# Kernel optimization log

Hardware: AMD Instinct MI355X
Metric: run time of the kernel (lower is better)

## Reference

```python
import jax, jax.numpy as jnp
import numpy as np

B, TQ, TKV, D, H = 2, 1024, 1024, 1024, 16
HD = D // H
BUCKETS, MAX_REL = 32, 128
SPAN = BUCKETS  # pos_ebd_size


def make_log_bucket_position(rel_pos, bucket_size, max_position):
    sign = jnp.sign(rel_pos)
    mid = bucket_size // 2
    abs_pos = jnp.where((rel_pos < mid) & (rel_pos > -mid), mid - 1, jnp.abs(rel_pos))
    log_pos = jnp.ceil(jnp.log(abs_pos.astype(jnp.float32) / mid)
                       / np.float32(np.log((max_position - 1) / mid)) * (mid - 1)) + mid
    return jnp.where(abs_pos <= mid, rel_pos, (log_pos * sign).astype(rel_pos.dtype))


def setup_inputs():
    key = jax.random.key(0)
    ks = jax.random.split(key, 12)
    s = 0.02
    f32 = jnp.float32
    return {
        "query_states": jax.random.normal(ks[0], (B, TQ, D), f32),
        "key_value_states": jax.random.normal(ks[1], (B, TKV, D), f32),
        "Wq": jax.random.normal(ks[2], (D, D), f32) * s, "bq": jnp.zeros((D,), f32),
        "Wk": jax.random.normal(ks[3], (D, D), f32) * s, "bk": jnp.zeros((D,), f32),
        "Wv": jax.random.normal(ks[4], (D, D), f32) * s, "bv": jnp.zeros((D,), f32),
        "Wo": jax.random.normal(ks[5], (D, D), f32) * s, "bo": jnp.zeros((D,), f32),
        "Wpk": jax.random.normal(ks[6], (D, D), f32) * s, "bpk": jnp.zeros((D,), f32),
        "Wpq": jax.random.normal(ks[7], (D, D), f32) * s, "bpq": jnp.zeros((D,), f32),
        "rel_emb": jax.random.normal(ks[8], (2 * SPAN, D), f32) * s,
        "ln_g": jnp.ones((D,), f32), "ln_b": jnp.zeros((D,), f32),
        "attention_mask": jnp.zeros((B, TKV), jnp.bool_),
    }


def reference(query_states, key_value_states, Wq, bq, Wk, bk, Wv, bv, Wo, bo,
              Wpk, bpk, Wpq, bpq, rel_emb, ln_g, ln_b, attention_mask):
    # projections -> [B,H,T,hd]
    q = (query_states @ Wq.T + bq).reshape(B, TQ, H, HD).transpose(0, 2, 1, 3)
    k = (key_value_states @ Wk.T + bk).reshape(B, TKV, H, HD).transpose(0, 2, 1, 3)
    v = (key_value_states @ Wv.T + bv).reshape(B, TKV, H, HD).transpose(0, 2, 1, 3)
    scale = jnp.sqrt(jnp.float32(HD * 3))  # scale_factor = 1 + c2p + p2c
    scores = jnp.einsum('bhqd,bhkd->bhqk', q, k) / scale

    # layer-normalized relative embeddings [2*SPAN, D]
    mu = rel_emb.mean(-1, keepdims=True)
    var = ((rel_emb - mu) ** 2).mean(-1, keepdims=True)
    re = (rel_emb - mu) * jax.lax.rsqrt(var + 1e-5) * ln_g + ln_b
    pos_k = (re @ Wpk.T + bpk).reshape(2 * SPAN, H, HD).transpose(1, 0, 2)  # [H,2S,hd]
    pos_q = (re @ Wpq.T + bpq).reshape(2 * SPAN, H, HD).transpose(1, 0, 2)

    rel = make_log_bucket_position(jnp.arange(TQ)[:, None] - jnp.arange(TKV)[None, :],
                                   BUCKETS, MAX_REL)                      # [Tq,Tkv]
    c2p_pos = jnp.clip(rel + SPAN, 0, 2 * SPAN - 1)
    p2c_pos = jnp.clip(-rel + SPAN, 0, 2 * SPAN - 1)
    pscale = jnp.sqrt(jnp.float32(HD * 2))

    # c2p: gather along relative-position axis
    c2p = jnp.einsum('bhqd,hpd->bhqp', q, pos_k)                          # [B,H,Tq,2S]
    iq = jnp.arange(TQ)[:, None]
    c2p_g = c2p[:, :, iq, c2p_pos]                                        # [B,H,Tq,Tkv]

    # p2c: gather then transpose (requires Tq == Tkv, as in original torch expand)
    p2c = jnp.einsum('bhkd,hpd->bhkp', k, pos_q)                          # [B,H,Tkv,2S]
    ik = jnp.arange(TKV)[:, None]
    p2c_g = p2c[:, :, ik, p2c_pos].transpose(0, 1, 3, 2)                  # [B,H,Tq,Tkv]

    scores = scores + c2p_g / pscale + p2c_g / pscale
    scores = jnp.where(attention_mask[:, None, None, :], -jnp.inf, scores)
    probs = jax.nn.softmax(scores.astype(jnp.float32), axis=-1).astype(q.dtype)

    ctx = jnp.einsum('bhqk,bhkd->bhqd', probs, v).transpose(0, 2, 1, 3).reshape(B, TQ, D)
    return ctx @ Wo.T + bo
```

## Files before the change

kernel.cpp:

```cpp
#include <hip/hip_runtime.h>
#include <hip/hip_bf16.h>
#include <math.h>

#define B   2
#define TQ  1024
#define TKV 1024
#define D   1024
#define H   16
#define HD  64
#define P   64
#define SPAN 32

#define NEG_INF (-3.0e38f)

typedef __attribute__((ext_vector_type(8))) short bf16x8;
typedef __attribute__((ext_vector_type(4))) float f32x4;
typedef unsigned short ushort_t;

static constexpr size_t RE_OFF   = 0;
static constexpr size_t POSK_OFF = (size_t)64 * 1024;
static constexpr size_t POSQ_OFF = (size_t)128 * 1024;
static constexpr size_t FLOATS_END = (size_t)192 * 1024;
static constexpr size_t SHORT_BASE_BYTES = FLOATS_END * 4;
static constexpr size_t C2P_S  = 0;
static constexpr size_t P2C_S  = (size_t)2 * 1024 * 1024;
static constexpr size_t QH_S   = (size_t)4 * 1024 * 1024;
static constexpr size_t QL_S   = (size_t)6 * 1024 * 1024;
static constexpr size_t KH_S   = (size_t)8 * 1024 * 1024;
static constexpr size_t KL_S   = (size_t)10 * 1024 * 1024;
static constexpr size_t VTH_S  = (size_t)12 * 1024 * 1024;
static constexpr size_t VTL_S  = (size_t)14 * 1024 * 1024;
static constexpr size_t CTXH_S = (size_t)16 * 1024 * 1024;
static constexpr size_t CTXL_S = (size_t)18 * 1024 * 1024;
static constexpr size_t AKVH_S = (size_t)20 * 1024 * 1024;
static constexpr size_t AKVL_S = (size_t)22 * 1024 * 1024;
static constexpr size_t TAB_OFF_BYTES = SHORT_BASE_BYTES + (size_t)24 * 1024 * 1024 * 2;

__device__ __forceinline__ void split2(float x, unsigned short& h, unsigned short& l) {
  unsigned int u = __float_as_uint(x);
  h = (unsigned short)(u >> 16);
  float r = x - __uint_as_float(u & 0xffff0000u);
  unsigned int v = __float_as_uint(r);
  v += 0x7fffu + ((v >> 16) & 1u);
  l = (unsigned short)(v >> 16);
}

__device__ __forceinline__ unsigned short bf16rn(float x) {
  unsigned int v = __float_as_uint(x);
  v += 0x7fffu + ((v >> 16) & 1u);
  return (unsigned short)(v >> 16);
}

__device__ __forceinline__ float bf2f(unsigned short u) {
  return __uint_as_float(((unsigned int)u) << 16);
}

__global__ __launch_bounds__(256) void fused_pre(const float* __restrict__ kv,
    ushort_t* __restrict__ oh, ushort_t* __restrict__ ol,
    const float* __restrict__ re_in, const float* __restrict__ ln_g,
    const float* __restrict__ ln_b, float* __restrict__ re_out,
    unsigned char* __restrict__ tab) {
  const int bid = blockIdx.x;
  const int tid = threadIdx.x;
  if (bid < 1024) {
    size_t i = ((size_t)bid * 256 + tid) * 8;
    float4 a = *(const float4*)&kv[i];
    float4 b = *(const float4*)&kv[i + 4];
    float xs[8] = {a.x, a.y, a.z, a.w, b.x, b.y, b.z, b.w};
    bf16x8 th, tl;
    #pragma unroll
    for (int j = 0; j < 8; j++) {
      unsigned short hh, ll;
      split2(xs[j], hh, ll);
      th[j] = (short)hh; tl[j] = (short)ll;
    }
    *(bf16x8*)&oh[i] = th;
    *(bf16x8*)&ol[i] = tl;
  } else if (bid < 1088) {
    const int row = bid - 1024;
    const float* xr = re_in + (size_t)row * D;
    __shared__ float red[4];
    float s = 0.f;
    for (int i = tid; i < D; i += 256) s += xr[i];
    #pragma unroll
    for (int off = 32; off; off >>= 1) s += __shfl_down(s, off);
    if ((tid & 63) == 0) red[tid >> 6] = s;
    __syncthreads();
    float mu = (red[0] + red[1] + red[2] + red[3]) * (1.0f / D);
    __syncthreads();
    float vs = 0.f;
    for (int i = tid; i < D; i += 256) { float dd = xr[i] - mu; vs += dd * dd; }
    #pragma unroll
    for (int off = 32; off; off >>= 1) vs += __shfl_down(vs, off);
    if ((tid & 63) == 0) red[tid >> 6] = vs;
    __syncthreads();
    float var = (red[0] + red[1] + red[2] + red[3]) * (1.0f / D);
    float rs = rsqrtf(var + 1e-5f);
    for (int i = tid; i < D; i += 256)
      re_out[(size_t)row * D + i] = (xr[i] - mu) * rs * ln_g[i] + ln_b[i];
  } else {
    int i = (bid - 1088) * 256 + tid;
    if (i >= 2047) return;
    int d = i - 1023;
    int ad = d < 0 ? -d : d;
    int bucket;
    if (ad <= 16) {
      bucket = d;
    } else {
      double x = log((double)ad / 16.0) / log(127.0 / 16.0) * 15.0;
      double xr = floor(x + 0.5);
      double xc = (fabs(x - xr) < 1e-9) ? xr : ceil(x);
      int li = (int)xc + 16;
      bucket = (d > 0) ? li : -li;
    }
    int t = bucket + SPAN;
    t = t < 0 ? 0 : (t > 63 ? 63 : t);
    tab[i] = (unsigned char)t;
  }
}

__global__ __launch_bounds__(256) void gemm_pos(const float* __restrict__ A,
    const float* __restrict__ W0, const float* __restrict__ b0, float* __restrict__ C0,
    const float* __restrict__ W1, const float* __restrict__ b1, float* __restrict__ C1) {
  const float* W = blockIdx.z ? W1 : W0;
  const float* bias = blockIdx.z ? b1 : b0;
  float* C = blockIdx.z ? C1 : C0;

  __shared__ short sAh[64 * 32], sAl[64 * 32], sBh[64 * 32], sBl[64 * 32];
  const int t = threadIdx.x;
  const int bn = blockIdx.x * 64;
  const int wid = t >> 6, lane = t & 63;
  const int wr = wid >> 1, wc = wid & 1;
  const int fr = lane & 15, fo = (lane >> 4) * 8;
  const int srow = t >> 3, scol = (t & 7) * 4;

  f32x4 acc[2][2];
  #pragma unroll
  for (int i = 0; i < 2; i++)
    #pragma unroll
    for (int j = 0; j < 2; j++) acc[i][j] = (f32x4){0.f, 0.f, 0.f, 0.f};

  float4 rA[2], rW[2];
  auto ld = [&](int k0) {
    #pragma unroll
    for (int i = 0; i < 2; i++) {
      rA[i] = *(const float4*)&A[(size_t)(srow + 32 * i) * 1024 + k0 + scol];
      rW[i] = *(const float4*)&W[(size_t)(bn + srow + 32 * i) * 1024 + k0 + scol];
    }
  };
  ld(0);

  for (int k0 = 0; k0 < 1024; k0 += 32) {
    __syncthreads();
    #pragma unroll
    for (int i = 0; i < 2; i++) {
      int row = srow + 32 * i;
      unsigned short h0,h1,h2,h3,l0,l1,l2,l3;
      split2(rA[i].x,h0,l0); split2(rA[i].y,h1,l1); split2(rA[i].z,h2,l2); split2(rA[i].w,h3,l3);
      *(short4*)&sAh[row * 32 + scol] = make_short4((short)h0,(short)h1,(short)h2,(short)h3);
      *(short4*)&sAl[row * 32 + scol] = make_short4((short)l0,(short)l1,(short)l2,(short)l3);
      split2(rW[i].x,h0,l0); split2(rW[i].y,h1,l1); split2(rW[i].z,h2,l2); split2(rW[i].w,h3,l3);
      *(short4*)&sBh[row * 32 + scol] = make_short4((short)h0,(short)h1,(short)h2,(short)h3);
      *(short4*)&sBl[row * 32 + scol] = make_short4((short)l0,(short)l1,(short)l2,(short)l3);
    }
    if (k0 + 32 < 1024) ld(k0 + 32);
    __syncthreads();

    bf16x8 ah[2], al[2], bh[2], bl[2];
    #pragma unroll
    for (int mf = 0; mf < 2; mf++) {
      int r = (wr * 32 + mf * 16 + fr) * 32 + fo;
      ah[mf] = *(const bf16x8*)&sAh[r];
      al[mf] = *(const bf16x8*)&sAl[r];
    }
    #pragma unroll
    for (int nf = 0; nf < 2; nf++) {
      int r = (wc * 32 + nf * 16 + fr) * 32 + fo;
      bh[nf] = *(const bf16x8*)&sBh[r];
      bl[nf] = *(const bf16x8*)&sBl[r];
    }
    #pragma unroll
    for (int mf = 0; mf < 2; mf++)
      #pragma unroll
      for (int nf = 0; nf < 2; nf++) {
        acc[mf][nf] = __builtin_amdgcn_mfma_f32_16x16x32_bf16(ah[mf], bh[nf], acc[mf][nf], 0, 0, 0);
        acc[mf][nf] = __builtin_amdgcn_mfma_f32_16x16x32_bf16(ah[mf], bl[nf], acc[mf][nf], 0, 0, 0);
        acc[mf][nf] = __builtin_amdgcn_mfma_f32_16x16x32_bf16(al[mf], bh[nf], acc[mf][nf], 0, 0, 0);
      }
  }

  #pragma unroll
  for (int mf = 0; mf < 2; mf++) {
    int rbase = wr * 32 + mf * 16 + (lane >> 4) * 4;
    #pragma unroll
    for (int nf = 0; nf < 2; nf++) {
      int col = bn + wc * 32 + nf * 16 + fr;
      float bb = bias[col];
      #pragma unroll
      for (int r = 0; r < 4; r++)
        C[(size_t)(rbase + r) * 1024 + col] = acc[mf][nf][r] + bb;
    }
  }
}

__global__ __launch_bounds__(256) void gemm_split(
    const float* __restrict__ Aq,
    const ushort_t* __restrict__ AKVH, const ushort_t* __restrict__ AKVL,
    const float* __restrict__ W0, const float* __restrict__ W1, const float* __restrict__ W2,
    const float* __restrict__ b0, const float* __restrict__ b1, const float* __restrict__ b2,
    ushort_t* __restrict__ QH_, ushort_t* __restrict__ QL_,
    ushort_t* __restrict__ KH_, ushort_t* __restrict__ KL_,
    ushort_t* __restrict__ VH_, ushort_t* __restrict__ VL_,
    int K) {
  const int z = blockIdx.z;
  const float* W = (z == 0) ? W0 : (z == 1) ? W1 : W2;
  const float* bias = (z == 0) ? b0 : (z == 1) ? b1 : b2;

  const int flat2 = blockIdx.y * 16 + blockIdx.x;
  const int x = flat2 & 7, w = flat2 >> 3;
  const int bm = ((x >> 1) * 4 + (w >> 3)) * 128;
  const int bn = ((x & 1) * 8 + (w & 7)) * 64;

  __shared__ short sAhi[128 * 32];
  __shared__ short sAlo[128 * 32];
  __shared__ short sBhi[64 * 32];
  __shared__ short sBlo[64 * 32];

  const int t = threadIdx.x;
  const int wid = t >> 6, lane = t & 63;
  const int wr = wid >> 1, wc = wid & 1;
  const int fr = lane & 15, g = lane >> 4;

  f32x4 acc[4][2];
  #pragma unroll
  for (int i = 0; i < 4; i++)
    #pragma unroll
    for (int j = 0; j < 2; j++)
      acc[i][j] = (f32x4){0.f, 0.f, 0.f, 0.f};

  const int srow = t >> 3;
  const int scol = (t & 7) * 4;
  const int ar = t >> 1;
  const int ac = (t & 1) * 16;

  float4 rA[4], rW[2];
  bf16x8 rAH[2], rAL[2];
  auto ld = [&](int k0) {
    if (z == 0) {
      #pragma unroll
      for (int i = 0; i < 4; i++)
        rA[i] = *(const float4*)&Aq[(size_t)(bm + srow + 32 * i) * K + k0 + scol];
    } else {
      const size_t abase = (size_t)(bm + ar) * K + k0 + ac;
      rAH[0] = *(const bf16x8*)&AKVH[abase];
      rAH[1] = *(const bf16x8*)&AKVH[abase + 8];
      rAL[0] = *(const bf16x8*)&AKVL[abase];
      rAL[1] = *(const bf16x8*)&AKVL[abase + 8];
    }
    #pragma unroll
    for (int i = 0; i < 2; i++)
      rW[i] = *(const float4*)&W[(size_t)(bn + srow + 32 * i) * K + k0 + scol];
  };
  ld(0);

  for (int k0 = 0; k0 < K; k0 += 32) {
    __syncthreads();
    if (z == 0) {
      #pragma unroll
      for (int i = 0; i < 4; i++) {
        int row = srow + 32 * i;
        int dst = ((row >> 4) * 4 + (scol >> 3)) * 128 + (row & 15) * 8 + (scol & 7);
        unsigned short h0, h1, h2, h3, l0, l1, l2, l3;
        split2(rA[i].x, h0, l0); split2(rA[i].y, h1, l1); split2(rA[i].z, h2, l2); split2(rA[i].w, h3, l3);
        *(short4*)&sAhi[dst] = make_short4((short)h0, (short)h1, (short)h2, (short)h3);
        *(short4*)&sAlo[dst] = make_short4((short)l0, (short)l1, (short)l2, (short)l3);
      }
    } else {
      const int g0 = ac >> 3;
      const int base0 = ((ar >> 4) * 4 + g0) * 128 + (ar & 15) * 8;
      const int base1 = ((ar >> 4) * 4 + g0 + 1) * 128 + (ar & 15) * 8;
      *(bf16x8*)&sAhi[base0] = rAH[0];
      *(bf16x8*)&sAhi[base1] = rAH[1];
      *(bf16x8*)&sAlo[base0] = rAL[0];
      *(bf16x8*)&sAlo[base1] = rAL[1];
    }
    #pragma unroll
    for (int i = 0; i < 2; i++) {
      int row = srow + 32 * i;
      int dst = ((row >> 4) * 4 + (scol >> 3)) * 128 + (row & 15) * 8 + (scol & 7);
      unsigned short h0, h1, h2, h3, l0, l1, l2, l3;
      split2(rW[i].x, h0, l0); split2(rW[i].y, h1, l1); split2(rW[i].z, h2, l2); split2(rW[i].w, h3, l3);
      *(short4*)&sBhi[dst] = make_short4((short)h0, (short)h1, (short)h2, (short)h3);
      *(short4*)&sBlo[dst] = make_short4((short)l0, (short)l1, (short)l2, (short)l3);
    }
    if (k0 + 32 < K) ld(k0 + 32);
    __syncthreads();

    bf16x8 ah[4], al[4], bh[2], bl[2];
    #pragma unroll
    for (int mf = 0; mf < 4; mf++) {
      int r = ((wr * 4 + mf) * 4 + g) * 128 + fr * 8;
      ah[mf] = *(const bf16x8*)&sAhi[r];
      al[mf] = *(const bf16x8*)&sAlo[r];
    }
    #pragma unroll
    for (int nf = 0; nf < 2; nf++) {
      int r = ((wc * 2 + nf) * 4 + g) * 128 + fr * 8;
      bh[nf] = *(const bf16x8*)&sBhi[r];
      bl[nf] = *(const bf16x8*)&sBlo[r];
    }
    #pragma unroll
    for (int mf = 0; mf < 4; mf++)
      #pragma unroll
      for (int nf = 0; nf < 2; nf++) {
        acc[mf][nf] = __builtin_amdgcn_mfma_f32_16x16x32_bf16(ah[mf], bh[nf], acc[mf][nf], 0, 0, 0);
        acc[mf][nf] = __builtin_amdgcn_mfma_f32_16x16x32_bf16(ah[mf], bl[nf], acc[mf][nf], 0, 0, 0);
        acc[mf][nf] = __builtin_amdgcn_mfma_f32_16x16x32_bf16(al[mf], bh[nf], acc[mf][nf], 0, 0, 0);
      }
  }

  if (z == 2) {
    #pragma unroll
    for (int mf = 0; mf < 4; mf++) {
      int m0 = bm + wr * 64 + mf * 16 + (lane >> 4) * 4;
      int bb2 = m0 >> 10, t0 = m0 & 1023;
      #pragma unroll
      for (int nf = 0; nf < 2; nf++) {
        int col = bn + wc * 32 + nf * 16 + fr;
        int hh = col >> 6, dd = col & 63;
        float bvv = bias[col];
        unsigned short h4[4], l4[4];
        #pragma unroll
        for (int r = 0; r < 4; r++) split2(acc[mf][nf][r] + bvv, h4[r], l4[r]);
        size_t dst = (((size_t)bb2 * 16 + hh) * 64 + dd) * 1024 + t0;
        *(short4*)&VH_[dst] = make_short4((short)h4[0], (short)h4[1], (short)h4[2], (short)h4[3]);
        *(short4*)&VL_[dst] = make_short4((short)l4[0], (short)l4[1], (short)l4[2], (short)l4[3]);
      }
    }
  } else {
    ushort_t* OH = (z == 0) ? QH_ : KH_;
    ushort_t* OL = (z == 0) ? QL_ : KL_;
    #pragma unroll
    for (int mf = 0; mf < 4; mf++) {
      int rbase = bm + wr * 64 + mf * 16 + (lane >> 4) * 4;
      #pragma unroll
      for (int nf = 0; nf < 2; nf++) {
        int col = bn + wc * 32 + nf * 16 + fr;
        float bb = bias[col];
        #pragma unroll
        for (int r = 0; r < 4; r++) {
          unsigned short hh, ll;
          split2(acc[mf][nf][r] + bb, hh, ll);
          OH[(size_t)(rbase + r) * 1024 + col] = hh;
          OL[(size_t)(rbase + r) * 1024 + col] = ll;
        }
      }
    }
  }
}

__global__ __launch_bounds__(256) void gemm_out(
    const ushort_t* __restrict__ AH, const ushort_t* __restrict__ AL,
    const float* __restrict__ W, const float* __restrict__ bias, float* __restrict__ C) {
  __shared__ short sAh[64 * 32], sAl[64 * 32], sBh[64 * 32], sBl[64 * 32];
  const int t = threadIdx.x;
  const int flat2 = blockIdx.y * 16 + blockIdx.x;
  const int x = flat2 & 7, w = flat2 >> 3;
  const int bm = ((x >> 1) * 8 + (w >> 3)) * 64;
  const int bn = ((x & 1) * 8 + (w & 7)) * 64;
  const int wid = t >> 6, lane = t & 63;
  const int wr = wid >> 1, wc = wid & 1;
  const int fr = lane & 15, g = lane >> 4;
  const int arow = t >> 2, achk = (t & 3) * 8;
  const int srow = t >> 3, scol = (t & 7) * 4;

  f32x4 acc[2][2];
  #pragma unroll
  for (int i = 0; i < 2; i++)
    #pragma unroll
    for (int j = 0; j < 2; j++) acc[i][j] = (f32x4){0.f, 0.f, 0.f, 0.f};

  bf16x8 rAH, rAL;
  float4 rW[2];
  auto ld = [&](int k0) {
    rAH = *(const bf16x8*)&AH[(size_t)(bm + arow) * 1024 + k0 + achk];
    rAL = *(const bf16x8*)&AL[(size_t)(bm + arow) * 1024 + k0 + achk];
    #pragma unroll
    for (int i = 0; i < 2; i++)
      rW[i] = *(const float4*)&W[(size_t)(bn + srow + 32 * i) * 1024 + k0 + scol];
  };
  ld(0);

  for (int k0 = 0; k0 < 1024; k0 += 32) {
    __syncthreads();
    {
      const int dstA = ((arow >> 4) * 4 + (achk >> 3)) * 128 + (arow & 15) * 8;
      *(bf16x8*)&sAh[dstA] = rAH;
      *(bf16x8*)&sAl[dstA] = rAL;
    }
    #pragma unroll
    for (int i = 0; i < 2; i++) {
      int row = srow + 32 * i;
      int dst = ((row >> 4) * 4 + (scol >> 3)) * 128 + (row & 15) * 8 + (scol & 7);
      unsigned short h0,h1,h2,h3,l0,l1,l2,l3;
      split2(rW[i].x,h0,l0); split2(rW[i].y,h1,l1); split2(rW[i].z,h2,l2); split2(rW[i].w,h3,l3);
      *(short4*)&sBh[dst] = make_short4((short)h0,(short)h1,(short)h2,(short)h3);
      *(short4*)&sBl[dst] = make_short4((short)l0,(short)l1,(short)l2,(short)l3);
    }
    if (k0 + 32 < 1024) ld(k0 + 32);
    __syncthreads();

    bf16x8 ah[2], al[2], bh[2], bl[2];
    #pragma unroll
    for (int mf = 0; mf < 2; mf++) {
      int r = ((wr * 2 + mf) * 4 + g) * 128 + fr * 8;
      ah[mf] = *(const bf16x8*)&sAh[r];
      al[mf] = *(const bf16x8*)&sAl[r];
    }
    #pragma unroll
    for (int nf = 0; nf < 2; nf++) {
      int r = ((wc * 2 + nf) * 4 + g) * 128 + fr * 8;
      bh[nf] = *(const bf16x8*)&sBh[r];
      bl[nf] = *(const bf16x8*)&sBl[r];
    }
    #pragma unroll
    for (int mf = 0; mf < 2; mf++)
      #pragma unroll
      for (int nf = 0; nf < 2; nf++) {
        acc[mf][nf] = __builtin_amdgcn_mfma_f32_16x16x32_bf16(ah[mf], bh[nf], acc[mf][nf], 0, 0, 0);
        acc[mf][nf] = __builtin_amdgcn_mfma_f32_16x16x32_bf16(ah[mf], bl[nf], acc[mf][nf], 0, 0, 0);
        acc[mf][nf] = __builtin_amdgcn_mfma_f32_16x16x32_bf16(al[mf], bh[nf], acc[mf][nf], 0, 0, 0);
      }
  }

  #pragma unroll
  for (int mf = 0; mf < 2; mf++) {
    int rbase = bm + wr * 32 + mf * 16 + (lane >> 4) * 4;
    #pragma unroll
    for (int nf = 0; nf < 2; nf++) {
      int col = bn + wc * 32 + nf * 16 + fr;
      float bb = bias[col];
      #pragma unroll
      for (int r = 0; r < 4; r++)
        C[(size_t)(rbase + r) * 1024 + col] = acc[mf][nf][r] + bb;
    }
  }
}

__global__ __launch_bounds__(256) void relproj_mfma(
    const ushort_t* __restrict__ QH, const ushort_t* __restrict__ QL,
    const ushort_t* __restrict__ KH, const ushort_t* __restrict__ KL,
    const float* __restrict__ POSK, const float* __restrict__ POSQ,
    ushort_t* __restrict__ O0, ushort_t* __restrict__ O1) {
  const int z = blockIdx.z;
  const ushort_t* XH = z ? KH : QH;
  const ushort_t* XL = z ? KL : QL;
  const float* POS = z ? POSQ : POSK;
  ushort_t* out = z ? O1 : O0;
  const int bh = blockIdx.y, b = bh >> 4, h = bh & 15;
  const int t0 = blockIdx.x * 256;

  const int tid = threadIdx.x;
  const int wid = tid >> 6, lane = tid & 63;
  const int g = lane >> 4, fr = lane & 15;

  __shared__ __align__(16) short sPh[4096], sPl[4096];
  {
    const int sr = tid >> 2;
    const int cb = (tid & 3) * 16;
    const float* pp = &POS[(size_t)sr * 1024 + h * HD + cb];
    #pragma unroll
    for (int o = 0; o < 16; o += 8) {
      float4 a = *(const float4*)(pp + o);
      float4 c = *(const float4*)(pp + o + 4);
      float xs[8] = {a.x, a.y, a.z, a.w, c.x, c.y, c.z, c.w};
      bf16x8 th, tl;
      #pragma unroll
      for (int j = 0; j < 8; j++) {
        unsigned short hh, ll;
        split2(xs[j], hh, ll);
        th[j] = (short)hh; tl[j] = (short)ll;
      }
      int d0 = cb + o;
      int addr = (((sr >> 4) * 8) + ((d0 >> 5) * 4) + ((d0 >> 3) & 3)) * 128 + (sr & 15) * 8;
      *(bf16x8*)&sPh[addr] = th;
      *(bf16x8*)&sPl[addr] = tl;
    }
  }
  __syncthreads();

  const float inv_ps = 0.08838834764831845f;
  f32x4 acc[4][4];
  #pragma unroll
  for (int mf = 0; mf < 4; mf++)
    #pragma unroll
    for (int nf = 0; nf < 4; nf++) acc[mf][nf] = (f32x4){0.f, 0.f, 0.f, 0.f};

  #pragma unroll
  for (int mf = 0; mf < 4; mf++) {
    const int trow = t0 + wid * 64 + mf * 16 + fr;
    const size_t xbase = ((size_t)b * TQ + trow) * D + h * HD;
    #pragma unroll
    for (int ks = 0; ks < 2; ks++) {
      bf16x8 ah = *(const bf16x8*)&XH[xbase + ks * 32 + g * 8];
      bf16x8 al = *(const bf16x8*)&XL[xbase + ks * 32 + g * 8];
      #pragma unroll
      for (int nf = 0; nf < 4; nf++) {
        bf16x8 bhf = *(const bf16x8*)&sPh[(nf * 8 + ks * 4 + g) * 128 + fr * 8];
        bf16x8 blf = *(const bf16x8*)&sPl[(nf * 8 + ks * 4 + g) * 128 + fr * 8];
        acc[mf][nf] = __builtin_amdgcn_mfma_f32_16x16x32_bf16(ah, bhf, acc[mf][nf], 0, 0, 0);
        acc[mf][nf] = __builtin_amdgcn_mfma_f32_16x16x32_bf16(ah, blf, acc[mf][nf], 0, 0, 0);
        acc[mf][nf] = __builtin_amdgcn_mfma_f32_16x16x32_bf16(al, bhf, acc[mf][nf], 0, 0, 0);
      }
    }
  }

  #pragma unroll
  for (int mf = 0; mf < 4; mf++) {
    #pragma unroll
    for (int nf = 0; nf < 4; nf++) {
      int p = nf * 16 + fr;
      #pragma unroll
      for (int rr = 0; rr < 4; rr++) {
        int tt = t0 + wid * 64 + mf * 16 + g * 4 + rr;
        out[((size_t)bh * TQ + tt) * P + p] = bf16rn(acc[mf][nf][rr] * inv_ps);
      }
    }
  }
}

__global__ __launch_bounds__(256, 3) void attn_mfma(
    const ushort_t* __restrict__ QHB, const ushort_t* __restrict__ QLB,
    const ushort_t* __restrict__ KH, const ushort_t* __restrict__ KL,
    const ushort_t* __restrict__ VTH, const ushort_t* __restrict__ VTL,
    const ushort_t* __restrict__ c2p, const ushort_t* __restrict__ p2c,
    const unsigned char* __restrict__ mask, const unsigned char* __restrict__ tab,
    ushort_t* __restrict__ CTXH, ushort_t* __restrict__ CTXL) {
  const int flat = blockIdx.y * gridDim.x + blockIdx.x;
  const int nid = (flat & 7) * 64 + (flat >> 3);
  const int bh = nid >> 4, b = bh >> 4, h = bh & 15;
  const int q0 = (nid & 15) * 64;

  const int tid = threadIdx.x;
  const int wid = tid >> 6, lane = tid & 63;
  const int g = lane >> 4, fr = lane & 15;

  __shared__ __align__(16) short sKh[4096], sKl[4096], sVh[4096], sVl[4096];
  __shared__ __align__(16) ushort_t sc2p[64][72];
  __shared__ __align__(16) ushort_t sp2c[64][72];
  __shared__ unsigned char stab[384];
  __shared__ unsigned char smask[64];

  bf16x8 qh[2], ql[2];
  {
    const int qrow = q0 + wid * 16 + fr;
    const size_t qidx = ((size_t)b * TQ + qrow) * D + h * HD + g * 8;
    #pragma unroll
    for (int ks = 0; ks < 2; ks++) {
      qh[ks] = *(const bf16x8*)&QHB[qidx + ks * 32];
      ql[ks] = *(const bf16x8*)&QLB[qidx + ks * 32];
    }
  }

  const int sr = tid >> 2;
  const int sj0 = tid & 3;
  const int smf = sr >> 4, sfr = sr & 15;
  const int cb = (tid & 3) * 16;
  const int qloc = wid * 16 + fr;

  {
    const ushort_t* cp = c2p + ((size_t)bh * TQ + q0 + sr) * P + cb;
    *(bf16x8*)&sc2p[sr][cb]     = *(const bf16x8*)cp;
    *(bf16x8*)&sc2p[sr][cb + 8] = *(const bf16x8*)(cp + 8);
  }
  if (tid < 192) {
    stab[tid] = tab[832 + tid];
    stab[tid + 192] = (tid + 192 < 384) ? tab[832 + tid + 192] : (unsigned char)0;
  }
  __syncthreads();
  const float c2p0  = bf2f(sc2p[qloc][0]);
  const float c2p63 = bf2f(sc2p[qloc][63]);

  f32x4 acc[4];
  #pragma unroll
  for (int nf = 0; nf < 4; nf++) acc[nf] = (f32x4){0.f, 0.f, 0.f, 0.f};
  float m_run = NEG_INF, l_run = 0.f;

  const float inv_s = 0.07216878364870323f;

  bf16x8 rKh[2], rKl[2], rVh[2], rVl[2], rP0, rP1;
  unsigned char rmask = 0;

  auto load_tile = [&](int kt) {
    const int k0n = kt * 64;
    const size_t kbase = ((size_t)b * TKV + k0n + sr) * D + h * HD;
    const size_t vbase = ((size_t)bh * HD + sr) * TKV + k0n;
    const ushort_t* pp = p2c + ((size_t)bh * TKV + k0n + sr) * P + cb;
    #pragma unroll
    for (int u = 0; u < 2; u++) {
      int jj = sj0 + u * 4;
      rKh[u] = *(const bf16x8*)(KH + kbase + jj * 8);
      rKl[u] = *(const bf16x8*)(KL + kbase + jj * 8);
      rVh[u] = *(const bf16x8*)(VTH + vbase + jj * 8);
      rVl[u] = *(const bf16x8*)(VTL + vbase + jj * 8);
    }
    rP0 = *(const bf16x8*)pp;
    rP1 = *(const bf16x8*)(pp + 8);
    if (tid < 64) rmask = mask[(size_t)b * TKV + k0n + tid];
  };

  load_tile(0);

  for (int kt = 0; kt < TKV / 64; kt++) {
    const int k0 = kt * 64;
    __syncthreads();
    #pragma unroll
    for (int u = 0; u < 2; u++) {
      int jj = sj0 + u * 4;
      int sub = smf * 8 + (jj >> 2) * 4 + (jj & 3);
      *(bf16x8*)&sKh[sub * 128 + sfr * 8] = rKh[u];
      *(bf16x8*)&sKl[sub * 128 + sfr * 8] = rKl[u];
      *(bf16x8*)&sVh[sub * 128 + sfr * 8] = rVh[u];
      *(bf16x8*)&sVl[sub * 128 + sfr * 8] = rVl[u];
    }
    *(bf16x8*)&sp2c[sr][cb]     = rP0;
    *(bf16x8*)&sp2c[sr][cb + 8] = rP1;
    if (tid < 64) smask[tid] = rmask;
    if (kt + 1 < TKV / 64) load_tile(kt + 1);
    __syncthreads();

    f32x4 st[4];
    #pragma unroll
    for (int mf = 0; mf < 4; mf++) st[mf] = (f32x4){0.f, 0.f, 0.f, 0.f};
    __builtin_amdgcn_s_setprio(1);
    #pragma unroll
    for (int mf = 0; mf < 4; mf++) {
      #pragma unroll
      for (int ks = 0; ks < 2; ks++) {
        bf16x8 kh = *(const bf16x8*)&sKh[(mf * 8 + ks * 4 + g) * 128 + fr * 8];
        bf16x8 kl = *(const bf16x8*)&sKl[(mf * 8 + ks * 4 + g) * 128 + fr * 8];
        st[mf] = __builtin_amdgcn_mfma_f32_16x16x32_bf16(kh, qh[ks], st[mf], 0, 0, 0);
        st[mf] = __builtin_amdgcn_mfma_f32_16x16x32_bf16(kh, ql[ks], st[mf], 0, 0, 0);
        st[mf] = __builtin_amdgcn_mfma_f32_16x16x32_bf16(kl, qh[ks], st[mf], 0, 0, 0);
      }
    }
    __builtin_amdgcn_s_setprio(0);

    const int dtile = q0 - k0;
    float pv[4][4];
    float lmax = NEG_INF;
    if (dtile >= 192 || dtile <= -192) {
      const int C = (dtile >= 192) ? 63 : 0;
      const float cbias = (dtile >= 192) ? c2p63 : c2p0;
      #pragma unroll
      for (int mf = 0; mf < 4; mf++) {
        #pragma unroll
        for (int rr = 0; rr < 4; rr++) {
          int kj = mf * 16 + g * 4 + rr;
          float v = st[mf][rr] * inv_s + (cbias + bf2f(sp2c[kj][C]));
          v = smask[kj] ? NEG_INF : v;
          pv[mf][rr] = v;
          lmax = fmaxf(lmax, v);
        }
      }
    } else {
      const int dqs = q0 + qloc - k0 + 191;
      const ushort_t* c2prow = &sc2p[qloc][0];
      #pragma unroll
      for (int mf = 0; mf < 4; mf++) {
        #pragma unroll
        for (int rr = 0; rr < 4; rr++) {
          int kj = mf * 16 + g * 4 + rr;
          int tbi = stab[dqs - kj];
          float v = st[mf][rr] * inv_s + (bf2f(c2prow[tbi]) + bf2f(sp2c[kj][tbi]));
          v = smask[kj] ? NEG_INF : v;
          pv[mf][rr] = v;
          lmax = fmaxf(lmax, v);
        }
      }
    }
    lmax = fmaxf(lmax, __shfl_xor(lmax, 16));
    lmax = fmaxf(lmax, __shfl_xor(lmax, 32));
    if (!__all(lmax <= m_run)) {
      float mnew = fmaxf(m_run, lmax);
      float fac = __expf(m_run - mnew);
      m_run = mnew;
      l_run *= fac;
      float facr[4];
      #pragma unroll
      for (int rr = 0; rr < 4; rr++) facr[rr] = __shfl(fac, g * 4 + rr);
      #pragma unroll
      for (int nf = 0; nf < 4; nf++)
        #pragma unroll
        for (int rr = 0; rr < 4; rr++) acc[nf][rr] *= facr[rr];
    }
    float psum = 0.f;
    #pragma unroll
    for (int mf = 0; mf < 4; mf++)
      #pragma unroll
      for (int rr = 0; rr < 4; rr++) {
        float e = __expf(pv[mf][rr] - m_run);
        pv[mf][rr] = e;
        psum += e;
      }
    psum += __shfl_xor(psum, 16);
    psum += __shfl_xor(psum, 32);
    l_run += psum;

    bf16x8 pa[2];
    #pragma unroll
    for (int ks = 0; ks < 2; ks++) {
      bf16x8 t;
      #pragma unroll
      for (int j = 0; j < 8; j++) {
        int src = ((2 * (g & 1) + (j >> 2)) << 4) | fr;
        float v0 = __shfl(pv[2 * ks][j & 3], src);
        float v1 = __shfl(pv[2 * ks + 1][j & 3], src);
        float pvv = (g >> 1) ? v1 : v0;
        t[j] = (short)bf16rn(pvv);
      }
      pa[ks] = t;
    }

    __builtin_amdgcn_s_setprio(1);
    #pragma unroll
    for (int nf = 0; nf < 4; nf++) {
      #pragma unroll
      for (int ks = 0; ks < 2; ks++) {
        bf16x8 vh = *(const bf16x8*)&sVh[(nf * 8 + ks * 4 + g) * 128 + fr * 8];
        bf16x8 vl = *(const bf16x8*)&sVl[(nf * 8 + ks * 4 + g) * 128 + fr * 8];
        acc[nf] = __builtin_amdgcn_mfma_f32_16x16x32_bf16(pa[ks], vh, acc[nf], 0, 0, 0);
        acc[nf] = __builtin_amdgcn_mfma_f32_16x16x32_bf16(pa[ks], vl, acc[nf], 0, 0, 0);
      }
    }
    __builtin_amdgcn_s_setprio(0);
  }

  float invl[4];
  #pragma unroll
  for (int rr = 0; rr < 4; rr++) invl[rr] = 1.0f / __shfl(l_run, g * 4 + rr);
  #pragma unroll
  for (int nf = 0; nf < 4; nf++) {
    #pragma unroll
    for (int rr = 0; rr < 4; rr++) {
      int qrow = q0 + wid * 16 + g * 4 + rr;
      int dcol = h * HD + nf * 16 + fr;
      size_t idx = ((size_t)b * TQ + qrow) * D + dcol;
      unsigned short hh, ll;
      split2(acc[nf][rr] * invl[rr], hh, ll);
      CTXH[idx] = hh;
      CTXL[idx] = ll;
    }
  }
}

extern "C" void kernel_launch(void* const* d_in, const int* in_sizes, int n_in,
                              void* d_out, int out_size, void* d_ws, size_t ws_size,
                              hipStream_t stream) {
  const float* query = (const float*)d_in[0];
  const float* kv    = (const float*)d_in[1];
  const float* Wq  = (const float*)d_in[2];   const float* bq  = (const float*)d_in[3];
  const float* Wk  = (const float*)d_in[4];   const float* bk  = (const float*)d_in[5];
  const float* Wv  = (const float*)d_in[6];   const float* bv  = (const float*)d_in[7];
  const float* Wo  = (const float*)d_in[8];   const float* bo  = (const float*)d_in[9];
  const float* Wpk = (const float*)d_in[10];  const float* bpk = (const float*)d_in[11];
  const float* Wpq = (const float*)d_in[12];  const float* bpq = (const float*)d_in[13];
  const float* rel_emb = (const float*)d_in[14];
  const float* ln_g = (const float*)d_in[15];
  const float* ln_b = (const float*)d_in[16];
  const unsigned char* amask = (const unsigned char*)d_in[17];

  float* ws = (float*)d_ws;
  float* rebuf   = ws + RE_OFF;
  float* poskbuf = ws + POSK_OFF;
  float* posqbuf = ws + POSQ_OFF;
  ushort_t* sbase = (ushort_t*)((char*)d_ws + SHORT_BASE_BYTES);
  ushort_t* c2pbuf = sbase + C2P_S;
  ushort_t* p2cbuf = sbase + P2C_S;
  ushort_t* QH   = sbase + QH_S;
  ushort_t* QL   = sbase + QL_S;
  ushort_t* KH   = sbase + KH_S;
  ushort_t* KL   = sbase + KL_S;
  ushort_t* VTH  = sbase + VTH_S;
  ushort_t* VTL  = sbase + VTL_S;
  ushort_t* CTXH = sbase + CTXH_S;
  ushort_t* CTXL = sbase + CTXL_S;
  ushort_t* AKVH = sbase + AKVH_S;
  ushort_t* AKVL = sbase + AKVL_S;
  unsigned char* tab = (unsigned char*)d_ws + TAB_OFF_BYTES;

  fused_pre<<<1096, 256, 0, stream>>>(kv, AKVH, AKVL, rel_emb, ln_g, ln_b, rebuf, tab);
  gemm_pos<<<dim3(16, 1, 2), 256, 0, stream>>>(rebuf, Wpk, bpk, poskbuf, Wpq, bpq, posqbuf);
  gemm_split<<<dim3(16, 16, 3), 256, 0, stream>>>(
      query, AKVH, AKVL,  Wq, Wk, Wv,  bq, bk, bv,
      QH, QL, KH, KL, VTH, VTL, 1024);
  relproj_mfma<<<dim3(4, 32, 2), 256, 0, stream>>>(
      QH, QL, KH, KL, poskbuf, posqbuf, c2pbuf, p2cbuf);
  attn_mfma<<<dim3(16, 32), 256, 0, stream>>>(QH, QL, KH, KL, VTH, VTL,
                                              c2pbuf, p2cbuf, amask, tab, CTXH, CTXL);
  gemm_out<<<dim3(16, 32), 256, 0, stream>>>(CTXH, CTXL, Wo, bo, (float*)d_out);
}
```

Before: 190.2 us.

## Split attention over KV halves with flash-decoding style merge kernel

Each attention block now handles half of the key/value range, doubling the grid from 512 to 1024 blocks, and writes unnormalized partial context plus running max and sum. A new merge kernel combines the two halves using log-sum-exp rescaling and writes the final context. The aim is to fill more compute units on the GPU with the extra parallelism, at the cost of an extra kernel launch, more global memory traffic for the partial results, and reuse of the AKV scratch buffers.

```diff
diff --git a/kernel.cpp b/kernel.cpp
--- a/kernel.cpp
+++ b/kernel.cpp
@@ -35,6 +35,7 @@
 static constexpr size_t AKVH_S = (size_t)20 * 1024 * 1024;
 static constexpr size_t AKVL_S = (size_t)22 * 1024 * 1024;
 static constexpr size_t TAB_OFF_BYTES = SHORT_BASE_BYTES + (size_t)24 * 1024 * 1024 * 2;
+static constexpr size_t PML_OFF_BYTES = TAB_OFF_BYTES + 4096;
 
 __device__ __forceinline__ void split2(float x, unsigned short& h, unsigned short& l) {
   unsigned int u = __float_as_uint(x);
@@ -535,11 +536,15 @@
     const ushort_t* __restrict__ VTH, const ushort_t* __restrict__ VTL,
     const ushort_t* __restrict__ c2p, const ushort_t* __restrict__ p2c,
     const unsigned char* __restrict__ mask, const unsigned char* __restrict__ tab,
-    ushort_t* __restrict__ CTXH, ushort_t* __restrict__ CTXL) {
-  const int flat = blockIdx.y * gridDim.x + blockIdx.x;
-  const int nid = (flat & 7) * 64 + (flat >> 3);
-  const int bh = nid >> 4, b = bh >> 4, h = bh & 15;
-  const int q0 = (nid & 15) * 64;
+    ushort_t* __restrict__ P0H, ushort_t* __restrict__ P0L,
+    ushort_t* __restrict__ P1H, ushort_t* __restrict__ P1L,
+    float* __restrict__ pml) {
+  const int flat = blockIdx.x;
+  const int nid = (flat & 7) * 128 + (flat >> 3);
+  const int bh = nid >> 5, b = bh >> 4, h = bh & 15;
+  const int q0 = ((nid >> 1) & 15) * 64;
+  const int kvh = nid & 1;
+  const int kt0 = kvh * 8, kt1 = kt0 + 8;
 
   const int tid = threadIdx.x;
   const int wid = tid >> 6, lane = tid & 63;
@@ -609,9 +614,9 @@
     if (tid < 64) rmask = mask[(size_t)b * TKV + k0n + tid];
   };
 
-  load_tile(0);
-
-  for (int kt = 0; kt < TKV / 64; kt++) {
+  load_tile(kt0);
+
+  for (int kt = kt0; kt < kt1; kt++) {
     const int k0 = kt * 64;
     __syncthreads();
     #pragma unroll
@@ -626,7 +631,7 @@
     *(bf16x8*)&sp2c[sr][cb]     = rP0;
     *(bf16x8*)&sp2c[sr][cb + 8] = rP1;
     if (tid < 64) smask[tid] = rmask;
-    if (kt + 1 < TKV / 64) load_tile(kt + 1);
+    if (kt + 1 < kt1) load_tile(kt + 1);
     __syncthreads();
 
     f32x4 st[4];
@@ -736,9 +741,13 @@
     __builtin_amdgcn_s_setprio(0);
   }
 
-  float invl[4];
-  #pragma unroll
-  for (int rr = 0; rr < 4; rr++) invl[rr] = 1.0f / __shfl(l_run, g * 4 + rr);
+  ushort_t* OH = kvh ? P1H : P0H;
+  ushort_t* OL = kvh ? P1L : P0L;
+  if (g == 0) {
+    int mi = ((kvh * 2 + b) * 16 + h) * 1024 + (q0 + qloc);
+    pml[mi] = m_run;
+    pml[65536 + mi] = l_run;
+  }
   #pragma unroll
   for (int nf = 0; nf < 4; nf++) {
     #pragma unroll
@@ -747,11 +756,44 @@
       int dcol = h * HD + nf * 16 + fr;
       size_t idx = ((size_t)b * TQ + qrow) * D + dcol;
       unsigned short hh, ll;
-      split2(acc[nf][rr] * invl[rr], hh, ll);
-      CTXH[idx] = hh;
-      CTXL[idx] = ll;
-    }
-  }
+      split2(acc[nf][rr], hh, ll);
+      OH[idx] = hh;
+      OL[idx] = ll;
+    }
+  }
+}
+
+__global__ __launch_bounds__(256) void attn_merge(
+    const ushort_t* __restrict__ P0H, const ushort_t* __restrict__ P0L,
+    ushort_t* __restrict__ P1H, ushort_t* __restrict__ P1L,
+    const float* __restrict__ pml) {
+  size_t i = ((size_t)blockIdx.x * 256 + threadIdx.x) * 8;
+  int rowid = (int)(i >> 10);
+  int b = rowid >> 10, qrow = rowid & 1023;
+  int h = (int)((i & 1023) >> 6);
+  int mi0 = ((0 * 2 + b) * 16 + h) * 1024 + qrow;
+  int mi1 = ((1 * 2 + b) * 16 + h) * 1024 + qrow;
+  float mA = pml[mi0], lA = pml[65536 + mi0];
+  float mB = pml[mi1], lB = pml[65536 + mi1];
+  float mm = fmaxf(mA, mB);
+  float aA = __expf(mA - mm), aB = __expf(mB - mm);
+  float dinv = 1.0f / (lA * aA + lB * aB);
+  bf16x8 h0 = *(const bf16x8*)&P0H[i];
+  bf16x8 l0 = *(const bf16x8*)&P0L[i];
+  bf16x8 h1 = *(const bf16x8*)&P1H[i];
+  bf16x8 l1 = *(const bf16x8*)&P1L[i];
+  bf16x8 oh, ol;
+  #pragma unroll
+  for (int j = 0; j < 8; j++) {
+    float p0 = bf2f((ushort_t)h0[j]) + bf2f((ushort_t)l0[j]);
+    float p1 = bf2f((ushort_t)h1[j]) + bf2f((ushort_t)l1[j]);
+    float o = (p0 * aA + p1 * aB) * dinv;
+    unsigned short hh, ll;
+    split2(o, hh, ll);
+    oh[j] = (short)hh; ol[j] = (short)ll;
+  }
+  *(bf16x8*)&P1H[i] = oh;
+  *(bf16x8*)&P1L[i] = ol;
 }
 
 extern "C" void kernel_launch(void* const* d_in, const int* in_sizes, int n_in,
@@ -788,6 +830,7 @@
   ushort_t* AKVH = sbase + AKVH_S;
   ushort_t* AKVL = sbase + AKVL_S;
   unsigned char* tab = (unsigned char*)d_ws + TAB_OFF_BYTES;
+  float* pml = (float*)((char*)d_ws + PML_OFF_BYTES);
 
   fused_pre<<<1096, 256, 0, stream>>>(kv, AKVH, AKVL, rel_emb, ln_g, ln_b, rebuf, tab);
   gemm_pos<<<dim3(16, 1, 2), 256, 0, stream>>>(rebuf, Wpk, bpk, poskbuf, Wpq, bpq, posqbuf);
@@ -796,7 +839,9 @@
       QH, QL, KH, KL, VTH, VTL, 1024);
   relproj_mfma<<<dim3(4, 32, 2), 256, 0, stream>>>(
       QH, QL, KH, KL, poskbuf, posqbuf, c2pbuf, p2cbuf);
-  attn_mfma<<<dim3(16, 32), 256, 0, stream>>>(QH, QL, KH, KL, VTH, VTL,
-                                              c2pbuf, p2cbuf, amask, tab, CTXH, CTXL);
+  attn_mfma<<<1024, 256, 0, stream>>>(QH, QL, KH, KL, VTH, VTL,
+                                      c2pbuf, p2cbuf, amask, tab,
+                                      AKVH, AKVL, CTXH, CTXL, pml);
+  attn_merge<<<1024, 256, 0, stream>>>(AKVH, AKVL, CTXH, CTXL, pml);
   gemm_out<<<dim3(16, 32), 256, 0, stream>>>(CTXH, CTXL, Wo, bo, (float*)d_out);
 }
```

After: 202.0 us. 1.06x slower.
